# Performance work log

Hardware: AMD Instinct MI355X
Metric: run time of the kernel (lower is better)

## Reference

```python
import jax, jax.numpy as jnp
import numpy as np

B, S, H, I = 2, 4096, 2048, 8192
K_RATIO = 0.5
K = int(K_RATIO * I)  # 4096 kept activations per token


def setup_inputs() -> dict:
    key = jax.random.key(0)
    kx, kg, ku, kd = jax.random.split(key, 4)
    x = jax.random.normal(kx, (B, S, H), dtype=jnp.float32)
    # nn.Linear(in, out, bias=False) weight has shape [out, in]; y = x @ W.T
    Wg = jax.random.normal(kg, (I, H), dtype=jnp.float32) * (1.0 / np.sqrt(H))
    Wu = jax.random.normal(ku, (I, H), dtype=jnp.float32) * (1.0 / np.sqrt(H))
    Wd = jax.random.normal(kd, (H, I), dtype=jnp.float32) * (1.0 / np.sqrt(I))
    return {"x": x, "Wg": Wg, "Wu": Wu, "Wd": Wd}


def topk_activation(g):
    # Keep top-K entries by magnitude along the last dim, zero the rest.
    ag = jnp.abs(g)
    kth = jax.lax.top_k(ag, K)[0][..., -1:]  # [B,S,1] k-th largest |g|
    return jnp.where(ag >= kth, g, jnp.zeros_like(g))


def reference(x, Wg, Wu, Wd):
    gate = topk_activation(jnp.einsum('bsh,ih->bsi', x, Wg))  # [B,S,I] sparse
    up = jnp.einsum('bsh,ih->bsi', x, Wu)                      # [B,S,I]
    return jnp.einsum('bsi,hi->bsh', gate * up, Wd)            # [B,S,H]
```

## Files before the change

kernel.cpp:

```cpp
#include <hip/hip_runtime.h>

#define T_TOK 8192
#define HDIM  2048
#define IDIM  8192
#define KKEEP 4096
#define TCHK  4096
#define BAND  1.6e-3f
#define MAXB  192

typedef _Float16 f16x8 __attribute__((ext_vector_type(8)));
typedef float    f32x4 __attribute__((ext_vector_type(4)));
typedef ushort   u16x8 __attribute__((ext_vector_type(8)));

#define AS1 __attribute__((address_space(1)))
#define AS3 __attribute__((address_space(3)))
#define BARR asm volatile("s_barrier" ::: "memory")

__device__ __forceinline__ int swzA(int b) {
    return b ^ ((b >> 3) & 0x30) ^ ((b >> 2) & 0x40);
}

union H16 { ushort u; _Float16 h; };


__global__ void cast_f16(const float4* __restrict__ in, ushort4* __restrict__ o, long n4) {
    long stride = (long)gridDim.x * blockDim.x;
    for (long i = (long)blockIdx.x * blockDim.x + threadIdx.x; i < n4; i += stride) {
        float4 v = in[i];
        float vv[4] = {v.x, v.y, v.z, v.w};
        union { _Float16 f[4]; ushort4 u; } H;
        #pragma unroll
        for (int j = 0; j < 4; ++j) H.f[j] = (_Float16)vv[j];
        o[i] = H.u;
    }
}

#define GLOAD(src_, dst_) \
    __builtin_amdgcn_global_load_lds((const AS1 void*)(src_), (AS3 void*)(dst_), 16, 0, 0)


#define STAGE4(pA_, pB_, kt_, buf_) do { \
    char* db_ = Lc + (buf_)*32768 + wave*1024; \
    GLOAD((pA_) + aBase + (kt_) + off0, db_); \
    GLOAD((pA_) + aBase + (kt_) + off1, db_ +  8192); \
    GLOAD((pB_) + bBase + (kt_) + off2, db_ + 16384); \
    GLOAD((pB_) + bBase + (kt_) + off3, db_ + 24576); \
  } while (0)

#define RDFRAG(dstA_, dstB_, tt_) do { \
    const char* bp_ = Lc + ((tt_) & 3) * 32768; \
    _Pragma("unroll") \
    for (int m_ = 0; m_ < 8; ++m_) (dstA_)[m_] = *(const f16x8*)(bp_ + pa + m_ * 1024); \
    _Pragma("unroll") \
    for (int n_ = 0; n_ < 4; ++n_) (dstB_)[n_] = *(const f16x8*)(bp_ + pb + n_ * 1024); \
  } while (0)

#define BODY_M(t_, curA_, curB_, nxtA_, nxtB_) do { \
    asm volatile("s_waitcnt vmcnt(4)" ::: "memory"); \
    BARR; \
    STAGE4(A0, B0, ((t_) + 3) << 5, ((t_) + 3) & 3); \
    RDFRAG(nxtA_, nxtB_, (t_) + 1); \
    _Pragma("unroll") \
    for (int m_ = 0; m_ < 8; ++m_) \
      _Pragma("unroll") \
      for (int n_ = 0; n_ < 4; ++n_) \
        acc[m_][n_] = __builtin_amdgcn_mfma_f32_16x16x32_f16((curA_)[m_], (curB_)[n_], acc[m_][n_], 0, 0, 0); \
    __builtin_amdgcn_sched_group_barrier(0x010, 4, 0); \
    _Pragma("unroll") \
    for (int g_ = 0; g_ < 4; ++g_) { \
      __builtin_amdgcn_sched_group_barrier(0x100, 3, 0); \
      __builtin_amdgcn_sched_group_barrier(0x008, 8, 0); \
    } \
  } while (0)

#define BODY_T(t_, curA_, curB_, nxtA_, nxtB_) do { \
    if ((t_) + 2 < NT) asm volatile("s_waitcnt vmcnt(4)" ::: "memory"); \
    else               asm volatile("s_waitcnt vmcnt(0)" ::: "memory"); \
    BARR; \
    if ((t_) + 3 < NT) STAGE4(A0, B0, ((t_) + 3) << 5, ((t_) + 3) & 3); \
    if ((t_) + 1 < NT) RDFRAG(nxtA_, nxtB_, (t_) + 1); \
    __builtin_amdgcn_s_setprio(1); \
    _Pragma("unroll") \
    for (int m_ = 0; m_ < 8; ++m_) \
      _Pragma("unroll") \
      for (int n_ = 0; n_ < 4; ++n_) \
        acc[m_][n_] = __builtin_amdgcn_mfma_f32_16x16x32_f16((curA_)[m_], (curB_)[n_], acc[m_][n_], 0, 0, 0); \
    __builtin_amdgcn_s_setprio(0); \
  } while (0)

template <int MODE>
__global__ __launch_bounds__(512, 2) void gemm4(
    const _Float16* __restrict__ A0, const _Float16* __restrict__ B0,
    int N, int Kp, float* __restrict__ Cf, _Float16* __restrict__ Ch)
{
    __shared__ __align__(128) char Lc[131072];
    const int tid  = threadIdx.x;
    const int lane = tid & 63;
    const int wave = tid >> 6;
    const int wr = wave >> 2, wc = wave & 3;

    const int gx = gridDim.x, gy = gridDim.y;
    const int nwg = gx * gy;
    const int orig = blockIdx.y * gx + blockIdx.x;
    const int q = nwg >> 3, r = nwg & 7, xcd = orig & 7, lid = orig >> 3;
    const int wg = (xcd < r ? xcd * (q + 1) : r * (q + 1) + (xcd - r) * q) + lid;
    const int bm = wg / gy, bn = wg % gy;

    int off0, off1, off2, off3;
    {
        int o[4];
        #pragma unroll
        for (int g = 0; g < 4; ++g) {
            int p = g * 8192 + tid * 16;
            int l = swzA(p);
            int row = (l >> 6) & 255;
            int col = (l & 63) >> 1;
            o[g] = row * Kp + col;
        }
        off0 = o[0]; off1 = o[1]; off2 = o[2]; off3 = o[3];
    }
    const size_t aBase = (size_t)bm * 256 * Kp;
    const size_t bBase = (size_t)bn * 256 * Kp;

    const int l15 = lane & 15, lhi = lane >> 4;
    const int pa = swzA((wr * 128 + l15) * 64 + lhi * 16);
    const int pb = swzA(16384 + (wc * 64 + l15) * 64 + lhi * 16);

    const int NT = Kp >> 5;
    f32x4 acc[8][4] = {};
    f16x8 a0f[8], b0f[4], a1f[8], b1f[4];

    STAGE4(A0, B0, 0,  0);
    STAGE4(A0, B0, 32, 1);
    STAGE4(A0, B0, 64, 2);
    asm volatile("s_waitcnt vmcnt(8)" ::: "memory");
    BARR;
    RDFRAG(a0f, b0f, 0);

    for (int t = 0; t + 5 < NT; t += 2) {
        BODY_M(t,     a0f, b0f, a1f, b1f);
        BODY_M(t + 1, a1f, b1f, a0f, b0f);
    }
    for (int t = NT - 4; t < NT; t += 2) {
        BODY_T(t,     a0f, b0f, a1f, b1f);
        BODY_T(t + 1, a1f, b1f, a0f, b0f);
    }

    const int r0 = bm * 256 + wr * 128 + (lane >> 4) * 4;
    const int c0 = bn * 256 + wc * 64 + (lane & 15);
    #pragma unroll
    for (int m = 0; m < 8; ++m) {
        #pragma unroll
        for (int n = 0; n < 4; ++n) {
            #pragma unroll
            for (int rr = 0; rr < 4; ++rr) {
                const size_t idx = (size_t)(r0 + m * 16 + rr) * N + (c0 + n * 16);
                if (MODE == 0) Cf[idx] = acc[m][n][rr];
                else           Ch[idx] = (_Float16)acc[m][n][rr];
            }
        }
    }
}


__global__ __launch_bounds__(256) void topk_sel(
    _Float16* __restrict__ GP, const _Float16* __restrict__ U,
    const float* __restrict__ xf, const float* __restrict__ Wgf)
{
    __shared__ ushort keys[IDIM];
    __shared__ float  xrow[HDIM];
    __shared__ unsigned char bmap[IDIM];
    __shared__ unsigned hist[256], sA_[256], sB_[256];
    __shared__ unsigned selBin, selAbove;
    __shared__ int Acnt, nbv;
    __shared__ int   bidxs[MAXB];
    __shared__ float bval[MAXB];
    __shared__ int   kflag[MAXB];

    const int tid = threadIdx.x;
    const int t = blockIdx.x;
    _Float16* grow = GP + (size_t)t * IDIM;
    const _Float16* urow = U + (size_t)t * IDIM;

    if (tid == 0) { Acnt = 0; nbv = 0; }
    for (int j8 = tid * 8; j8 < IDIM; j8 += 2048) {
        u16x8 v = *(const u16x8*)(grow + j8);
        u16x8 k;
        #pragma unroll
        for (int e = 0; e < 8; ++e) k[e] = (ushort)(v[e] & 0x7FFFu);
        *(u16x8*)(keys + j8) = k;
    }
    for (int j4 = tid; j4 < IDIM / 4; j4 += 256)
        ((unsigned*)bmap)[j4] = 0xFFFFFFFFu;
    for (int j4 = tid * 4; j4 < HDIM; j4 += 1024)
        *(float4*)(xrow + j4) = *(const float4*)(xf + (size_t)t * HDIM + j4);
    __syncthreads();

    unsigned kq = 0;
    int Krem = KKEEP;
    for (int pass = 0; pass < 2; ++pass) {
        const int shift = pass == 0 ? 7 : 0;
        const unsigned msk = pass == 0 ? 255u : 127u;
        hist[tid] = 0;
        __syncthreads();
        for (int j8 = tid * 8; j8 < IDIM; j8 += 2048) {
            u16x8 kv = *(const u16x8*)(keys + j8);
            #pragma unroll
            for (int e = 0; e < 8; ++e) {
                unsigned k = kv[e];
                bool ok = (pass == 0) || ((k >> 7) == (kq >> 7));
                if (ok) atomicAdd(&hist[(k >> shift) & msk], 1u);
            }
        }
        __syncthreads();
        sA_[tid] = hist[tid];
        __syncthreads();
        unsigned *src = sA_, *dst = sB_;
        for (int off = 1; off < 256; off <<= 1) {
            unsigned v = src[tid] + ((tid + off < 256) ? src[tid + off] : 0u);
            dst[tid] = v;
            __syncthreads();
            unsigned* tmp = src; src = dst; dst = tmp;
        }
        unsigned S  = src[tid];
        unsigned Sn = (tid < 255) ? src[tid + 1] : 0u;
        if ((int)S >= Krem && (int)Sn < Krem) { selBin = (unsigned)tid; selAbove = Sn; }
        __syncthreads();
        kq |= selBin << shift;
        Krem -= (int)selAbove;
        __syncthreads();
    }
    H16 cv; cv.u = (ushort)kq;
    const float kthf = (float)cv.h;
    const float hif = kthf + BAND;
    const float lof = kthf - BAND;

    for (int j8 = tid * 8; j8 < IDIM; j8 += 2048) {
        u16x8 kv = *(const u16x8*)(keys + j8);
        #pragma unroll
        for (int e = 0; e < 8; ++e) {
            H16 c; c.u = kv[e];
            float v = (float)c.h;
            if (v > hif) atomicAdd(&Acnt, 1);
            else if (v >= lof) {
                int s = atomicAdd(&nbv, 1);
                if (s < MAXB) { bidxs[s] = j8 + e; bmap[j8 + e] = (unsigned char)s; }
            }
        }
    }
    __syncthreads();

    const int nbc = nbv < MAXB ? nbv : MAXB;
    int R = KKEEP - Acnt;
    R = R < 0 ? 0 : (R > nbc ? nbc : R);

    const int wv = tid >> 6, ln = tid & 63;
    for (int j = wv; j < nbc; j += 4) {
        const float* wrow = Wgf + (size_t)bidxs[j] * HDIM;
        float s = 0.f;
        #pragma unroll
        for (int it = 0; it < HDIM / 256; ++it) {
            const int c = it * 256 + ln * 4;
            float4 w = *(const float4*)(wrow + c);
            float4 xv = *(const float4*)(xrow + c);
            s = fmaf(xv.x, w.x, s);
            s = fmaf(xv.y, w.y, s);
            s = fmaf(xv.z, w.z, s);
            s = fmaf(xv.w, w.w, s);
        }
        #pragma unroll
        for (int o = 32; o; o >>= 1) s += __shfl_xor(s, o);
        if (ln == 0) bval[j] = fabsf(s);
    }
    __syncthreads();

    for (int j = tid; j < nbc; j += 256) {
        int rk = 0;
        float vj = bval[j];
        for (int k = 0; k < nbc; ++k) rk += (bval[k] > vj);
        kflag[j] = (rk < R) ? 1 : 0;
    }
    __syncthreads();

    for (int j8 = tid * 8; j8 < IDIM; j8 += 2048) {
        u16x8 g8 = *(const u16x8*)(grow + j8);
        u16x8 u8 = *(const u16x8*)(urow + j8);
        u16x8 p8;
        #pragma unroll
        for (int e = 0; e < 8; ++e) {
            H16 cg; cg.u = g8[e];
            H16 cu; cu.u = u8[e];
            float g = (float)cg.h;
            float v = fabsf(g);
            bool keep;
            unsigned char s = bmap[j8 + e];
            if (s != 255)      keep = (kflag[s] != 0);
            else if (v > hif)  keep = true;
            else if (v < lof)  keep = false;
            else               keep = (v >= kthf);
            H16 cp; cp.h = keep ? (_Float16)(g * (float)cu.h) : (_Float16)0.f;
            p8[e] = cp.u;
        }
        *(u16x8*)(grow + j8) = p8;
    }
}


extern "C" void kernel_launch(void* const* d_in, const int* in_sizes, int n_in,
                              void* d_out, int out_size, void* d_ws, size_t ws_size,
                              hipStream_t stream) {
    const float* x  = (const float*)d_in[0];
    const float* Wg = (const float*)d_in[1];
    const float* Wu = (const float*)d_in[2];
    const float* Wd = (const float*)d_in[3];

    const size_t NE   = (size_t)T_TOK * HDIM;
    const size_t szH2 = NE * 2;

    char* ws = (char*)d_ws;
    _Float16* xh   = (_Float16*)ws;
    _Float16* Wgh  = (_Float16*)(ws + szH2);
    _Float16* Wu16 = (_Float16*)(ws + 2 * szH2);
    _Float16* Wd16 = (_Float16*)(ws + 3 * szH2);
    _Float16* G    = (_Float16*)(ws + 4 * szH2);
    _Float16* Uc   = (_Float16*)d_out;

    const long n4 = (long)(NE / 4);
    cast_f16<<<1024, 256, 0, stream>>>((const float4*)x,  (ushort4*)xh,   n4);
    cast_f16<<<1024, 256, 0, stream>>>((const float4*)Wg, (ushort4*)Wgh,  n4);
    cast_f16<<<1024, 256, 0, stream>>>((const float4*)Wu, (ushort4*)Wu16, n4);
    cast_f16<<<1024, 256, 0, stream>>>((const float4*)Wd, (ushort4*)Wd16, n4);

    gemm4<1><<<dim3(T_TOK / 256, IDIM / 256), 512, 0, stream>>>(
        xh, Wgh, IDIM, HDIM, nullptr, G);

    for (int c0 = 0; c0 < T_TOK; c0 += TCHK) {
        gemm4<1><<<dim3(TCHK / 256, IDIM / 256), 512, 0, stream>>>(
            xh + (size_t)c0 * HDIM, Wu16, IDIM, HDIM, nullptr, Uc);
        topk_sel<<<TCHK, 256, 0, stream>>>(
            G + (size_t)c0 * IDIM, Uc, x + (size_t)c0 * HDIM, Wg);
    }

    gemm4<0><<<dim3(T_TOK / 256, HDIM / 256), 512, 0, stream>>>(
        G, Wd16, HDIM, IDIM, (float*)d_out, nullptr);
}
```

Baseline: 1.225 ms.

## Batch gate and up GEMMs per chunk and merge four cast kernels

Replaces the separate full gate GEMM and per-chunk up GEMM with one batched kernel per token chunk. Each workgroup picks gate or up weights by the low bit of its remapped index, so both tiles sharing the same x rows run in the same wave of workgroups. The four fp32-to-fp16 cast launches are merged into one launch with a 2D grid. This aims to improve L2 reuse of x, give each launch more workgroups and cut launch overhead, at the cost of interleaving two weight streams and launching half as many cast blocks per tensor.

```diff
diff --git a/kernel.cpp b/kernel.cpp
--- a/kernel.cpp
+++ b/kernel.cpp
@@ -23,7 +23,17 @@
 union H16 { ushort u; _Float16 h; };
 
 
-__global__ void cast_f16(const float4* __restrict__ in, ushort4* __restrict__ o, long n4) {
+__global__ void cast_all(const float4* __restrict__ x,  const float4* __restrict__ wg,
+                         const float4* __restrict__ wu, const float4* __restrict__ wd,
+                         ushort4* __restrict__ xo,  ushort4* __restrict__ wgo,
+                         ushort4* __restrict__ wuo, ushort4* __restrict__ wdo, long n4) {
+    const float4* in; ushort4* out;
+    switch (blockIdx.y) {
+        case 0:  in = x;  out = xo;  break;
+        case 1:  in = wg; out = wgo; break;
+        case 2:  in = wu; out = wuo; break;
+        default: in = wd; out = wdo; break;
+    }
     long stride = (long)gridDim.x * blockDim.x;
     for (long i = (long)blockIdx.x * blockDim.x + threadIdx.x; i < n4; i += stride) {
         float4 v = in[i];
@@ -31,7 +41,7 @@
         union { _Float16 f[4]; ushort4 u; } H;
         #pragma unroll
         for (int j = 0; j < 4; ++j) H.f[j] = (_Float16)vv[j];
-        o[i] = H.u;
+        out[i] = H.u;
     }
 }
 
@@ -55,10 +65,10 @@
     for (int n_ = 0; n_ < 4; ++n_) (dstB_)[n_] = *(const f16x8*)(bp_ + pb + n_ * 1024); \
   } while (0)
 
-#define BODY_M(t_, curA_, curB_, nxtA_, nxtB_) do { \
+#define BODY_M(pA_, pB_, t_, curA_, curB_, nxtA_, nxtB_) do { \
     asm volatile("s_waitcnt vmcnt(4)" ::: "memory"); \
     BARR; \
-    STAGE4(A0, B0, ((t_) + 3) << 5, ((t_) + 3) & 3); \
+    STAGE4(pA_, pB_, ((t_) + 3) << 5, ((t_) + 3) & 3); \
     RDFRAG(nxtA_, nxtB_, (t_) + 1); \
     _Pragma("unroll") \
     for (int m_ = 0; m_ < 8; ++m_) \
@@ -73,11 +83,11 @@
     } \
   } while (0)
 
-#define BODY_T(t_, curA_, curB_, nxtA_, nxtB_) do { \
+#define BODY_T(pA_, pB_, t_, curA_, curB_, nxtA_, nxtB_) do { \
     if ((t_) + 2 < NT) asm volatile("s_waitcnt vmcnt(4)" ::: "memory"); \
     else               asm volatile("s_waitcnt vmcnt(0)" ::: "memory"); \
     BARR; \
-    if ((t_) + 3 < NT) STAGE4(A0, B0, ((t_) + 3) << 5, ((t_) + 3) & 3); \
+    if ((t_) + 3 < NT) STAGE4(pA_, pB_, ((t_) + 3) << 5, ((t_) + 3) & 3); \
     if ((t_) + 1 < NT) RDFRAG(nxtA_, nxtB_, (t_) + 1); \
     __builtin_amdgcn_s_setprio(1); \
     _Pragma("unroll") \
@@ -88,16 +98,51 @@
     __builtin_amdgcn_s_setprio(0); \
   } while (0)
 
+#define GEMM_SETUP \
+    const int tid  = threadIdx.x; \
+    const int lane = tid & 63; \
+    const int wave = tid >> 6; \
+    const int wr = wave >> 2, wc = wave & 3; \
+    int off0, off1, off2, off3; \
+    { \
+        int o[4]; \
+        _Pragma("unroll") \
+        for (int g = 0; g < 4; ++g) { \
+            int p = g * 8192 + tid * 16; \
+            int l = swzA(p); \
+            int row = (l >> 6) & 255; \
+            int col = (l & 63) >> 1; \
+            o[g] = row * Kp + col; \
+        } \
+        off0 = o[0]; off1 = o[1]; off2 = o[2]; off3 = o[3]; \
+    } \
+    const int l15 = lane & 15, lhi = lane >> 4; \
+    const int pa = swzA((wr * 128 + l15) * 64 + lhi * 16); \
+    const int pb = swzA(16384 + (wc * 64 + l15) * 64 + lhi * 16);
+
+#define GEMM_KLOOP(pA_, pB_) \
+    STAGE4(pA_, pB_, 0,  0); \
+    STAGE4(pA_, pB_, 32, 1); \
+    STAGE4(pA_, pB_, 64, 2); \
+    asm volatile("s_waitcnt vmcnt(8)" ::: "memory"); \
+    BARR; \
+    RDFRAG(a0f, b0f, 0); \
+    for (int t = 0; t + 5 < NT; t += 2) { \
+        BODY_M(pA_, pB_, t,     a0f, b0f, a1f, b1f); \
+        BODY_M(pA_, pB_, t + 1, a1f, b1f, a0f, b0f); \
+    } \
+    for (int t = NT - 4; t < NT; t += 2) { \
+        BODY_T(pA_, pB_, t,     a0f, b0f, a1f, b1f); \
+        BODY_T(pA_, pB_, t + 1, a1f, b1f, a0f, b0f); \
+    }
+
 template <int MODE>
 __global__ __launch_bounds__(512, 2) void gemm4(
     const _Float16* __restrict__ A0, const _Float16* __restrict__ B0,
     int N, int Kp, float* __restrict__ Cf, _Float16* __restrict__ Ch)
 {
     __shared__ __align__(128) char Lc[131072];
-    const int tid  = threadIdx.x;
-    const int lane = tid & 63;
-    const int wave = tid >> 6;
-    const int wr = wave >> 2, wc = wave & 3;
+    GEMM_SETUP;
 
     const int gx = gridDim.x, gy = gridDim.y;
     const int nwg = gx * gy;
@@ -106,60 +151,67 @@
     const int wg = (xcd < r ? xcd * (q + 1) : r * (q + 1) + (xcd - r) * q) + lid;
     const int bm = wg / gy, bn = wg % gy;
 
-    int off0, off1, off2, off3;
-    {
-        int o[4];
-        #pragma unroll
-        for (int g = 0; g < 4; ++g) {
-            int p = g * 8192 + tid * 16;
-            int l = swzA(p);
-            int row = (l >> 6) & 255;
-            int col = (l & 63) >> 1;
-            o[g] = row * Kp + col;
-        }
-        off0 = o[0]; off1 = o[1]; off2 = o[2]; off3 = o[3];
-    }
     const size_t aBase = (size_t)bm * 256 * Kp;
     const size_t bBase = (size_t)bn * 256 * Kp;
-
-    const int l15 = lane & 15, lhi = lane >> 4;
-    const int pa = swzA((wr * 128 + l15) * 64 + lhi * 16);
-    const int pb = swzA(16384 + (wc * 64 + l15) * 64 + lhi * 16);
 
     const int NT = Kp >> 5;
     f32x4 acc[8][4] = {};
     f16x8 a0f[8], b0f[4], a1f[8], b1f[4];
 
-    STAGE4(A0, B0, 0,  0);
-    STAGE4(A0, B0, 32, 1);
-    STAGE4(A0, B0, 64, 2);
-    asm volatile("s_waitcnt vmcnt(8)" ::: "memory");
-    BARR;
-    RDFRAG(a0f, b0f, 0);
-
-    for (int t = 0; t + 5 < NT; t += 2) {
-        BODY_M(t,     a0f, b0f, a1f, b1f);
-        BODY_M(t + 1, a1f, b1f, a0f, b0f);
-    }
-    for (int t = NT - 4; t < NT; t += 2) {
-        BODY_T(t,     a0f, b0f, a1f, b1f);
-        BODY_T(t + 1, a1f, b1f, a0f, b0f);
-    }
+    GEMM_KLOOP(A0, B0);
 
     const int r0 = bm * 256 + wr * 128 + (lane >> 4) * 4;
     const int c0 = bn * 256 + wc * 64 + (lane & 15);
     #pragma unroll
-    for (int m = 0; m < 8; ++m) {
-        #pragma unroll
-        for (int n = 0; n < 4; ++n) {
+    for (int m = 0; m < 8; ++m)
+        #pragma unroll
+        for (int n = 0; n < 4; ++n)
             #pragma unroll
             for (int rr = 0; rr < 4; ++rr) {
                 const size_t idx = (size_t)(r0 + m * 16 + rr) * N + (c0 + n * 16);
                 if (MODE == 0) Cf[idx] = acc[m][n][rr];
                 else           Ch[idx] = (_Float16)acc[m][n][rr];
             }
-        }
-    }
+}
+
+__global__ __launch_bounds__(512, 2) void gemm4z(
+    const _Float16* __restrict__ A0, const _Float16* __restrict__ Bg,
+    const _Float16* __restrict__ Bu, int N, int Kp,
+    _Float16* __restrict__ Gout, _Float16* __restrict__ Uout)
+{
+    __shared__ __align__(128) char Lc[131072];
+    GEMM_SETUP;
+
+    const int nwg = gridDim.x;
+    const int orig = blockIdx.x;
+    const int q = nwg >> 3, r = nwg & 7, xcd = orig & 7, lid = orig >> 3;
+    const int wg = (xcd < r ? xcd * (q + 1) : r * (q + 1) + (xcd - r) * q) + lid;
+    const int z = wg & 1;
+    const int rest = wg >> 1;
+    const int gy = N / 256;
+    const int bm = rest / gy, bn = rest % gy;
+
+    const _Float16* B0 = z ? Bu : Bg;
+    _Float16* Ch = z ? Uout : Gout;
+
+    const size_t aBase = (size_t)bm * 256 * Kp;
+    const size_t bBase = (size_t)bn * 256 * Kp;
+
+    const int NT = Kp >> 5;
+    f32x4 acc[8][4] = {};
+    f16x8 a0f[8], b0f[4], a1f[8], b1f[4];
+
+    GEMM_KLOOP(A0, B0);
+
+    const int r0 = bm * 256 + wr * 128 + (lane >> 4) * 4;
+    const int c0 = bn * 256 + wc * 64 + (lane & 15);
+    #pragma unroll
+    for (int m = 0; m < 8; ++m)
+        #pragma unroll
+        for (int n = 0; n < 4; ++n)
+            #pragma unroll
+            for (int rr = 0; rr < 4; ++rr)
+                Ch[(size_t)(r0 + m * 16 + rr) * N + (c0 + n * 16)] = (_Float16)acc[m][n][rr];
 }
 
 
@@ -326,17 +378,15 @@
     _Float16* Uc   = (_Float16*)d_out;
 
     const long n4 = (long)(NE / 4);
-    cast_f16<<<1024, 256, 0, stream>>>((const float4*)x,  (ushort4*)xh,   n4);
-    cast_f16<<<1024, 256, 0, stream>>>((const float4*)Wg, (ushort4*)Wgh,  n4);
-    cast_f16<<<1024, 256, 0, stream>>>((const float4*)Wu, (ushort4*)Wu16, n4);
-    cast_f16<<<1024, 256, 0, stream>>>((const float4*)Wd, (ushort4*)Wd16, n4);
-
-    gemm4<1><<<dim3(T_TOK / 256, IDIM / 256), 512, 0, stream>>>(
-        xh, Wgh, IDIM, HDIM, nullptr, G);
+    cast_all<<<dim3(512, 4), 256, 0, stream>>>(
+        (const float4*)x, (const float4*)Wg, (const float4*)Wu, (const float4*)Wd,
+        (ushort4*)xh, (ushort4*)Wgh, (ushort4*)Wu16, (ushort4*)Wd16, n4);
 
     for (int c0 = 0; c0 < T_TOK; c0 += TCHK) {
-        gemm4<1><<<dim3(TCHK / 256, IDIM / 256), 512, 0, stream>>>(
-            xh + (size_t)c0 * HDIM, Wu16, IDIM, HDIM, nullptr, Uc);
+        const int nwg = 2 * (TCHK / 256) * (IDIM / 256);
+        gemm4z<<<dim3(nwg), 512, 0, stream>>>(
+            xh + (size_t)c0 * HDIM, Wgh, Wu16, IDIM, HDIM,
+            G + (size_t)c0 * IDIM, Uc);
         topk_sel<<<TCHK, 256, 0, stream>>>(
             G + (size_t)c0 * IDIM, Uc, x + (size_t)c0 * HDIM, Wg);
     }
```

Measured after the change: 1.202 ms. No clear change (-1.9%).
